# Optimization experiments

Measured on AMD Instinct MI355X. Metric: run time of the kernel, lower is better.

## Reference

```python
import jax, jax.numpy as jnp
import numpy as np
import math

NUM_LANDMARKS = 64
HEAD_DIM = 64
NUM_HEAD = 16
BATCH = 4
SEQ_LEN = 4096


def iterative_inv(mat, n_iter=6):
    # mat: [..., m, m]
    I = jnp.eye(mat.shape[-1], dtype=mat.dtype)
    K = mat
    # scalar normalization: global max of column sums * global max of row sums
    scale = 1.0 / (jnp.max(jnp.sum(jnp.abs(K), axis=-2)) * jnp.max(jnp.sum(jnp.abs(K), axis=-1)))
    V = scale * jnp.swapaxes(K, -1, -2)
    for _ in range(n_iter):
        KV = jnp.matmul(K, V)
        V = jnp.matmul(0.25 * V, 13.0 * I - jnp.matmul(KV, 15.0 * I - jnp.matmul(KV, 7.0 * I - KV)))
    return V


def setup_inputs() -> dict:
    key = jax.random.key(0)
    k1, k2, k3 = jax.random.split(key, 3)
    shape = (BATCH, NUM_HEAD, SEQ_LEN, HEAD_DIM)
    Q = jax.random.normal(k1, shape, dtype=jnp.float32)
    K = jax.random.normal(k2, shape, dtype=jnp.float32)
    V = jax.random.normal(k3, shape, dtype=jnp.float32)
    return {"Q": Q, "K": K, "V": V}


def reference(Q, K, V):
    seq_len = Q.shape[-2]
    m = NUM_LANDMARKS
    scale = 1.0 / math.sqrt(math.sqrt(HEAD_DIM))
    Q = Q * scale
    K = K * scale
    # landmark pooling: mean over contiguous segments of length seq_len // m
    seg = seq_len // m
    Q_lm = Q.reshape(-1, NUM_HEAD, m, seg, HEAD_DIM).mean(axis=-2)  # [B,H,m,d]
    K_lm = K.reshape(-1, NUM_HEAD, m, seg, HEAD_DIM).mean(axis=-2)  # [B,H,m,d]
    # three softmax kernels
    kernel_1 = jax.nn.softmax(jnp.einsum('bhsd,bhmd->bhsm', Q, K_lm), axis=-1)   # [B,H,S,m]
    kernel_2 = jax.nn.softmax(jnp.einsum('bhmd,bhnd->bhmn', Q_lm, K_lm), axis=-1)  # [B,H,m,m]
    kernel_3 = jax.nn.softmax(jnp.einsum('bhmd,bhsd->bhms', Q_lm, K), axis=-1)   # [B,H,m,S]
    inv_k2 = iterative_inv(kernel_2)
    X = jnp.matmul(jnp.matmul(kernel_1, inv_k2), jnp.matmul(kernel_3, V))  # [B,H,S,d]
    return X
```

## Files before the change

### kernel.cpp

```cpp
#include <hip/hip_runtime.h>
#include <hip/hip_bf16.h>

#define PAD 68
#define KP  72
#define SCALE 0.35355339059327379f

typedef __attribute__((ext_vector_type(8))) short bf16x8;
typedef __attribute__((ext_vector_type(4))) float f32x4;
#define MFMA_BF16 __builtin_amdgcn_mfma_f32_16x16x32_bf16

__device__ __forceinline__ short f2b(float f) {
    unsigned u = __float_as_uint(f);
    u += 0x7fff + ((u >> 16) & 1);
    return (short)(u >> 16);
}
__device__ __forceinline__ float b2f(short h) {
    return __uint_as_float(((unsigned)(unsigned short)h) << 16);
}

__device__ __forceinline__ void fma16(float acc[16], float a, const float* b) {
    const float4* b4 = reinterpret_cast<const float4*>(b);
    float4 x0 = b4[0], x1 = b4[1], x2 = b4[2], x3 = b4[3];
    acc[0]  += a * x0.x; acc[1]  += a * x0.y; acc[2]  += a * x0.z; acc[3]  += a * x0.w;
    acc[4]  += a * x1.x; acc[5]  += a * x1.y; acc[6]  += a * x1.z; acc[7]  += a * x1.w;
    acc[8]  += a * x2.x; acc[9]  += a * x2.y; acc[10] += a * x2.z; acc[11] += a * x2.w;
    acc[12] += a * x3.x; acc[13] += a * x3.y; acc[14] += a * x3.z; acc[15] += a * x3.w;
}

__device__ __forceinline__ int SWI(int row, int colS) {
    return (((row << 7) + (colS << 1)) ^ ((row & 7) << 4)) >> 1;
}

__global__ __launch_bounds__(256) void pool_kernel(const float* __restrict__ Q,
                                                   const float* __restrict__ K,
                                                   float* __restrict__ Qlm,
                                                   float* __restrict__ Klm,
                                                   short* __restrict__ Qlm_b,
                                                   short* __restrict__ Klm_b) {
    __shared__ float4 red[256];
    const int blk = blockIdx.x;
    const int t = threadIdx.x;
    const int d4 = t & 15;
    const int rg = t >> 4;
    const float4* Q4 = reinterpret_cast<const float4*>(Q);
    const float4* K4 = reinterpret_cast<const float4*>(K);

    float4 sQ = {0.f, 0.f, 0.f, 0.f}, sK = {0.f, 0.f, 0.f, 0.f};
#pragma unroll
    for (int rr = 0; rr < 4; rr++) {
        int row = blk * 64 + rg * 4 + rr;
        int off4 = (row << 4) + d4;
        float4 q = Q4[off4], k = K4[off4];
        sQ.x += q.x; sQ.y += q.y; sQ.z += q.z; sQ.w += q.w;
        sK.x += k.x; sK.y += k.y; sK.z += k.z; sK.w += k.w;
    }
    const float c = SCALE * (1.0f / 64.0f);
    red[t] = sQ;
    __syncthreads();
    if (t < 16) {
        float4 s = {0.f, 0.f, 0.f, 0.f};
#pragma unroll
        for (int g = 0; g < 16; g++) {
            float4 v = red[g * 16 + t];
            s.x += v.x; s.y += v.y; s.z += v.z; s.w += v.w;
        }
        s.x *= c; s.y *= c; s.z *= c; s.w *= c;
        reinterpret_cast<float4*>(Qlm + blk * 64)[t] = s;
        ushort4 ub = { (unsigned short)f2b(s.x), (unsigned short)f2b(s.y),
                       (unsigned short)f2b(s.z), (unsigned short)f2b(s.w) };
        *reinterpret_cast<ushort4*>(&Qlm_b[blk * 64 + t * 4]) = ub;
    }
    __syncthreads();
    red[t] = sK;
    __syncthreads();
    if (t < 16) {
        float4 s = {0.f, 0.f, 0.f, 0.f};
#pragma unroll
        for (int g = 0; g < 16; g++) {
            float4 v = red[g * 16 + t];
            s.x += v.x; s.y += v.y; s.z += v.z; s.w += v.w;
        }
        s.x *= c; s.y *= c; s.z *= c; s.w *= c;
        reinterpret_cast<float4*>(Klm + blk * 64)[t] = s;
        ushort4 ub = { (unsigned short)f2b(s.x), (unsigned short)f2b(s.y),
                       (unsigned short)f2b(s.z), (unsigned short)f2b(s.w) };
        *reinterpret_cast<ushort4*>(&Klm_b[blk * 64 + t * 4]) = ub;
    }
}

__global__ __launch_bounds__(256) void k2_kernel(const float* __restrict__ Qlm,
                                                 const float* __restrict__ Klm,
                                                 float* __restrict__ K2g,
                                                 unsigned* __restrict__ colmax) {
    __shared__ float Ql[64 * PAD], Kl[64 * PAD], S2[64 * PAD];
    const int bh = blockIdx.x, t = threadIdx.x;
#pragma unroll
    for (int n = 0; n < 16; n++) {
        int f = t + n * 256;
        Ql[(f >> 6) * PAD + (f & 63)] = Qlm[bh * 4096 + f];
        Kl[(f >> 6) * PAD + (f & 63)] = Klm[bh * 4096 + f];
    }
    __syncthreads();
    const int i = t >> 2, j0 = (t & 3) * 16;
    float acc[16];
#pragma unroll
    for (int u = 0; u < 16; u++) acc[u] = 0.f;
    const float4* Ql4 = reinterpret_cast<const float4*>(Ql);
    const float4* Kl4 = reinterpret_cast<const float4*>(Kl);
    for (int k4 = 0; k4 < 16; k4++) {
        float4 a = Ql4[i * 17 + k4];
#pragma unroll
        for (int u = 0; u < 16; u++) {
            float4 b = Kl4[(j0 + u) * 17 + k4];
            acc[u] += a.x * b.x + a.y * b.y + a.z * b.z + a.w * b.w;
        }
    }
#pragma unroll
    for (int u = 0; u < 16; u++) S2[i * PAD + j0 + u] = acc[u];
    __syncthreads();
    if (t < 64) {
        float m = -1e30f;
        for (int j = 0; j < 64; j++) m = fmaxf(m, S2[t * PAD + j]);
        float sum = 0.f;
        for (int j = 0; j < 64; j++) {
            float e = __expf(S2[t * PAD + j] - m);
            S2[t * PAD + j] = e; sum += e;
        }
        float inv = 1.0f / sum;
        for (int j = 0; j < 64; j++) S2[t * PAD + j] *= inv;
    }
    __syncthreads();
#pragma unroll
    for (int n = 0; n < 16; n++) {
        int f = t + n * 256;
        K2g[bh * 4096 + f] = S2[(f >> 6) * PAD + (f & 63)];
    }
    if (t < 64) {
        float c = 0.f;
        for (int ii = 0; ii < 64; ii++) c += S2[ii * PAD + t];
        atomicMax(colmax, __float_as_uint(c));
    }
}

__global__ __launch_bounds__(256) void fused_inv_k3v(const short* __restrict__ Qlm_b,
                                                     const float* __restrict__ K,
                                                     const float* __restrict__ V,
                                                     float* __restrict__ W2acc,
                                                     float* __restrict__ rowsum3,
                                                     const float* __restrict__ K2g,
                                                     const unsigned* __restrict__ colmax,
                                                     float* __restrict__ K2invg) {
    __shared__ __align__(16) char smem[65536];
    const int t = threadIdx.x;
    const int w = t >> 6, lane = t & 63, quad = lane >> 4, l15 = lane & 15;

    if (blockIdx.x < 64) {
        short* Krh = reinterpret_cast<short*>(smem);
        short* Krl = Krh + 4096;
        short* Ath = Krl + 4096;
        short* Atl = Ath + 4096;
        short* B1h = Atl + 4096;
        short* B1l = B1h + 4096;
        short* B2h = B1l + 4096;
        short* B2l = B2h + 4096;
        const int bh = blockIdx.x;
        const float scv = 1.0f / __uint_as_float(*colmax);
        const float* Kg = K2g + bh * 4096;

#pragma unroll
        for (int n = 0; n < 4; n++) {
            int f4 = t + n * 256;
            int r = f4 >> 4, c0 = (f4 & 15) * 4;
            float4 kk = *reinterpret_cast<const float4*>(Kg + r * 64 + c0);
            short h0 = f2b(kk.x), h1 = f2b(kk.y), h2 = f2b(kk.z), h3 = f2b(kk.w);
            ushort4 uh = {(unsigned short)h0, (unsigned short)h1,
                          (unsigned short)h2, (unsigned short)h3};
            ushort4 ul = {(unsigned short)f2b(kk.x - b2f(h0)), (unsigned short)f2b(kk.y - b2f(h1)),
                          (unsigned short)f2b(kk.z - b2f(h2)), (unsigned short)f2b(kk.w - b2f(h3))};
            *reinterpret_cast<ushort4*>(&Krh[SWI(r, c0)]) = uh;
            *reinterpret_cast<ushort4*>(&Krl[SWI(r, c0)]) = ul;
            float s0 = scv * kk.x, s1 = scv * kk.y, s2 = scv * kk.z, s3 = scv * kk.w;
            short g0 = f2b(s0), g1 = f2b(s1), g2 = f2b(s2), g3 = f2b(s3);
            ushort4 vh = {(unsigned short)g0, (unsigned short)g1,
                          (unsigned short)g2, (unsigned short)g3};
            ushort4 vl = {(unsigned short)f2b(s0 - b2f(g0)), (unsigned short)f2b(s1 - b2f(g1)),
                          (unsigned short)f2b(s2 - b2f(g2)), (unsigned short)f2b(s3 - b2f(g3))};
            *reinterpret_cast<ushort4*>(&B1h[SWI(r, c0)]) = vh;
            *reinterpret_cast<ushort4*>(&B1l[SWI(r, c0)]) = vl;
            float t0 = scv * Kg[(c0 + 0) * 64 + r];
            float t1 = scv * Kg[(c0 + 1) * 64 + r];
            float t2 = scv * Kg[(c0 + 2) * 64 + r];
            float t3 = scv * Kg[(c0 + 3) * 64 + r];
            short e0 = f2b(t0), e1 = f2b(t1), e2 = f2b(t2), e3 = f2b(t3);
            ushort4 th = {(unsigned short)e0, (unsigned short)e1,
                          (unsigned short)e2, (unsigned short)e3};
            ushort4 tl = {(unsigned short)f2b(t0 - b2f(e0)), (unsigned short)f2b(t1 - b2f(e1)),
                          (unsigned short)f2b(t2 - b2f(e2)), (unsigned short)f2b(t3 - b2f(e3))};
            *reinterpret_cast<ushort4*>(&B2h[SWI(r, c0)]) = th;
            *reinterpret_cast<ushort4*>(&B2l[SWI(r, c0)]) = tl;
        }
        float vreg[4][4];
#pragma unroll
        for (int nt = 0; nt < 4; nt++) {
            float4 vv = *reinterpret_cast<const float4*>(
                Kg + (nt * 16 + l15) * 64 + w * 16 + quad * 4);
            vreg[nt][0] = scv * vv.x; vreg[nt][1] = scv * vv.y;
            vreg[nt][2] = scv * vv.z; vreg[nt][3] = scv * vv.w;
        }
        __syncthreads();

#define LOADA(Lh, Ll) \
        bf16x8 ah0 = *reinterpret_cast<const bf16x8*>(&Lh[SWI(w * 16 + l15, quad * 8)]); \
        bf16x8 ah1 = *reinterpret_cast<const bf16x8*>(&Lh[SWI(w * 16 + l15, quad * 8 + 32)]); \
        bf16x8 al0 = *reinterpret_cast<const bf16x8*>(&Ll[SWI(w * 16 + l15, quad * 8)]); \
        bf16x8 al1 = *reinterpret_cast<const bf16x8*>(&Ll[SWI(w * 16 + l15, quad * 8 + 32)]);
#define PRODNT(Bh, Bl, nt, c) { \
        bf16x8 bh0 = *reinterpret_cast<const bf16x8*>(&Bh[SWI(nt * 16 + l15, quad * 8)]); \
        bf16x8 bh1 = *reinterpret_cast<const bf16x8*>(&Bh[SWI(nt * 16 + l15, quad * 8 + 32)]); \
        bf16x8 bl0 = *reinterpret_cast<const bf16x8*>(&Bl[SWI(nt * 16 + l15, quad * 8)]); \
        bf16x8 bl1 = *reinterpret_cast<const bf16x8*>(&Bl[SWI(nt * 16 + l15, quad * 8 + 32)]); \
        c = MFMA_BF16(ah0, bh0, c, 0, 0, 0); c = MFMA_BF16(ah1, bh1, c, 0, 0, 0); \
        c = MFMA_BF16(ah0, bl0, c, 0, 0, 0); c = MFMA_BF16(ah1, bl1, c, 0, 0, 0); \
        c = MFMA_BF16(al0, bh0, c, 0, 0, 0); c = MFMA_BF16(al1, bh1, c, 0, 0, 0); \
        c = MFMA_BF16(al0, bl0, c, 0, 0, 0); c = MFMA_BF16(al1, bl1, c, 0, 0, 0); }

        for (int iter = 0; iter < 6; iter++) {
            {
                LOADA(Krh, Krl)
#pragma unroll
                for (int nt = 0; nt < 4; nt++) {
                    f32x4 c = {0.f, 0.f, 0.f, 0.f};
                    PRODNT(B1h, B1l, nt, c)
                    short h0 = f2b(c[0]), h1 = f2b(c[1]), h2 = f2b(c[2]), h3 = f2b(c[3]);
                    ushort4 uh = {(unsigned short)h0, (unsigned short)h1,
                                  (unsigned short)h2, (unsigned short)h3};
                    ushort4 ul = {(unsigned short)f2b(c[0] - b2f(h0)),
                                  (unsigned short)f2b(c[1] - b2f(h1)),
                                  (unsigned short)f2b(c[2] - b2f(h2)),
                                  (unsigned short)f2b(c[3] - b2f(h3))};
                    *reinterpret_cast<ushort4*>(&Ath[SWI(nt * 16 + l15, w * 16 + quad * 4)]) = uh;
                    *reinterpret_cast<ushort4*>(&Atl[SWI(nt * 16 + l15, w * 16 + quad * 4)]) = ul;
                }
            }
            __syncthreads();
            float p[4][4];
            {
                LOADA(B2h, B2l)
#pragma unroll
                for (int nt = 0; nt < 4; nt++) {
                    f32x4 c = {0.f, 0.f, 0.f, 0.f};
                    PRODNT(Ath, Atl, nt, c)
#pragma unroll
                    for (int reg = 0; reg < 4; reg++) {
                        p[nt][reg] = c[reg];
                        short hh = f2b(c[reg]);
                        B1h[SWI(w * 16 + quad * 4 + reg, nt * 16 + l15)] = hh;
                        B1l[SWI(w * 16 + quad * 4 + reg, nt * 16 + l15)] = f2b(c[reg] - b2f(hh));
                    }
                }
            }
            __syncthreads();
            float q[4][4];
            {
                LOADA(B1h, B1l)
#pragma unroll
                for (int nt = 0; nt < 4; nt++) {
                    f32x4 c = {0.f, 0.f, 0.f, 0.f};
                    PRODNT(Ath, Atl, nt, c)
#pragma unroll
                    for (int reg = 0; reg < 4; reg++) {
                        q[nt][reg] = c[reg];
                        short hh = f2b(c[reg]);
                        B2h[SWI(w * 16 + quad * 4 + reg, nt * 16 + l15)] = hh;
                        B2l[SWI(w * 16 + quad * 4 + reg, nt * 16 + l15)] = f2b(c[reg] - b2f(hh));
                    }
                }
            }
            __syncthreads();
            {
                LOADA(B2h, B2l)
#pragma unroll
                for (int nt = 0; nt < 4; nt++) {
                    f32x4 c = {0.f, 0.f, 0.f, 0.f};
                    PRODNT(Ath, Atl, nt, c)
#pragma unroll
                    for (int reg = 0; reg < 4; reg++)
                        vreg[nt][reg] = 0.25f * (13.f * vreg[nt][reg] - 15.f * p[nt][reg]
                                                 + 7.f * q[nt][reg] - c[reg]);
                }
            }
#pragma unroll
            for (int nt = 0; nt < 4; nt++) {
                short h0 = f2b(vreg[nt][0]), h1 = f2b(vreg[nt][1]);
                short h2 = f2b(vreg[nt][2]), h3 = f2b(vreg[nt][3]);
                short g0 = f2b(vreg[nt][0] - b2f(h0)), g1 = f2b(vreg[nt][1] - b2f(h1));
                short g2 = f2b(vreg[nt][2] - b2f(h2)), g3 = f2b(vreg[nt][3] - b2f(h3));
                ushort4 uh = {(unsigned short)h0, (unsigned short)h1,
                              (unsigned short)h2, (unsigned short)h3};
                ushort4 ul = {(unsigned short)g0, (unsigned short)g1,
                              (unsigned short)g2, (unsigned short)g3};
                *reinterpret_cast<ushort4*>(&B1h[SWI(nt * 16 + l15, w * 16 + quad * 4)]) = uh;
                *reinterpret_cast<ushort4*>(&B1l[SWI(nt * 16 + l15, w * 16 + quad * 4)]) = ul;
                B2h[SWI(w * 16 + quad * 4 + 0, nt * 16 + l15)] = h0;
                B2h[SWI(w * 16 + quad * 4 + 1, nt * 16 + l15)] = h1;
                B2h[SWI(w * 16 + quad * 4 + 2, nt * 16 + l15)] = h2;
                B2h[SWI(w * 16 + quad * 4 + 3, nt * 16 + l15)] = h3;
                B2l[SWI(w * 16 + quad * 4 + 0, nt * 16 + l15)] = g0;
                B2l[SWI(w * 16 + quad * 4 + 1, nt * 16 + l15)] = g1;
                B2l[SWI(w * 16 + quad * 4 + 2, nt * 16 + l15)] = g2;
                B2l[SWI(w * 16 + quad * 4 + 3, nt * 16 + l15)] = g3;
            }
            __syncthreads();
        }
#undef LOADA
#undef PRODNT
#pragma unroll
        for (int nt = 0; nt < 4; nt++)
#pragma unroll
            for (int reg = 0; reg < 4; reg++)
                K2invg[bh * 4096 + (w * 16 + quad * 4 + reg) * 64 + nt * 16 + l15] =
                    vreg[nt][reg];
        return;
    }

    short* Kt = reinterpret_cast<short*>(smem);
    short* Vt = Kt + 64 * KP;
    short* Eb = Vt + 64 * KP;
    const int idx = blockIdx.x - 64;
    const int chunk = idx & 31, bh = idx >> 5;
    const float4* K4 = reinterpret_cast<const float4*>(K);
    const float4* V4 = reinterpret_cast<const float4*>(V);
    const int dg = t & 15;
    const int kr = t >> 4;
    const int bhBase = bh * 4096;

    const bf16x8* Qb = reinterpret_cast<const bf16x8*>(Qlm_b + bh * 4096);
    bf16x8 a0 = Qb[(w * 16 + l15) * 8 + quad];
    bf16x8 a1 = Qb[(w * 16 + l15) * 8 + quad + 4];

    f32x4 oacc[4];
    float rsum[4];
#pragma unroll
    for (int nt = 0; nt < 4; nt++) { oacc[nt] = (f32x4){0.f, 0.f, 0.f, 0.f}; rsum[nt] = 0.f; }

    const int sb0 = chunk * 128;
    for (int tile = 0; tile < 2; tile++) {
        const int sb = sb0 + tile * 64;
        __syncthreads();
#pragma unroll
        for (int n = 0; n < 4; n++) {
            float4 kk = K4[(bhBase + sb + kr + 16 * n) * 16 + dg];
            ushort4 uk = { (unsigned short)f2b(SCALE * kk.x), (unsigned short)f2b(SCALE * kk.y),
                           (unsigned short)f2b(SCALE * kk.z), (unsigned short)f2b(SCALE * kk.w) };
            *reinterpret_cast<ushort4*>(&Kt[(kr + 16 * n) * KP + dg * 4]) = uk;
        }
        {
            float4 pv0 = V4[(bhBase + sb + kr * 4 + 0) * 16 + dg];
            float4 pv1 = V4[(bhBase + sb + kr * 4 + 1) * 16 + dg];
            float4 pv2 = V4[(bhBase + sb + kr * 4 + 2) * 16 + dg];
            float4 pv3 = V4[(bhBase + sb + kr * 4 + 3) * 16 + dg];
            ushort4 u0 = { (unsigned short)f2b(pv0.x), (unsigned short)f2b(pv1.x),
                           (unsigned short)f2b(pv2.x), (unsigned short)f2b(pv3.x) };
            ushort4 u1 = { (unsigned short)f2b(pv0.y), (unsigned short)f2b(pv1.y),
                           (unsigned short)f2b(pv2.y), (unsigned short)f2b(pv3.y) };
            ushort4 u2 = { (unsigned short)f2b(pv0.z), (unsigned short)f2b(pv1.z),
                           (unsigned short)f2b(pv2.z), (unsigned short)f2b(pv3.z) };
            ushort4 u3 = { (unsigned short)f2b(pv0.w), (unsigned short)f2b(pv1.w),
                           (unsigned short)f2b(pv2.w), (unsigned short)f2b(pv3.w) };
            *reinterpret_cast<ushort4*>(&Vt[(dg * 4 + 0) * KP + kr * 4]) = u0;
            *reinterpret_cast<ushort4*>(&Vt[(dg * 4 + 1) * KP + kr * 4]) = u1;
            *reinterpret_cast<ushort4*>(&Vt[(dg * 4 + 2) * KP + kr * 4]) = u2;
            *reinterpret_cast<ushort4*>(&Vt[(dg * 4 + 3) * KP + kr * 4]) = u3;
        }
        __syncthreads();
#pragma unroll
        for (int nt = 0; nt < 4; nt++) {
            bf16x8 b0 = *reinterpret_cast<const bf16x8*>(&Kt[(nt * 16 + l15) * KP + quad * 8]);
            bf16x8 b1 = *reinterpret_cast<const bf16x8*>(&Kt[(nt * 16 + l15) * KP + quad * 8 + 32]);
            f32x4 c = {0.f, 0.f, 0.f, 0.f};
            c = MFMA_BF16(a0, b0, c, 0, 0, 0);
            c = MFMA_BF16(a1, b1, c, 0, 0, 0);
#pragma unroll
            for (int reg = 0; reg < 4; reg++) {
                float e = __expf(c[reg]);
                rsum[reg] += e;
                Eb[(w * 16 + quad * 4 + reg) * KP + nt * 16 + l15] = f2b(e);
            }
        }
        bf16x8 e0 = *reinterpret_cast<const bf16x8*>(&Eb[(w * 16 + l15) * KP + quad * 8]);
        bf16x8 e1 = *reinterpret_cast<const bf16x8*>(&Eb[(w * 16 + l15) * KP + quad * 8 + 32]);
#pragma unroll
        for (int nt = 0; nt < 4; nt++) {
            bf16x8 b0 = *reinterpret_cast<const bf16x8*>(&Vt[(nt * 16 + l15) * KP + quad * 8]);
            bf16x8 b1 = *reinterpret_cast<const bf16x8*>(&Vt[(nt * 16 + l15) * KP + quad * 8 + 32]);
            oacc[nt] = MFMA_BF16(e0, b0, oacc[nt], 0, 0, 0);
            oacc[nt] = MFMA_BF16(e1, b1, oacc[nt], 0, 0, 0);
        }
    }
#pragma unroll
    for (int reg = 0; reg < 4; reg++) {
        float s = rsum[reg];
        s += __shfl_xor(s, 1); s += __shfl_xor(s, 2);
        s += __shfl_xor(s, 4); s += __shfl_xor(s, 8);
        rsum[reg] = s;
    }
    const int row0 = w * 16 + quad * 4;
    if (l15 == 0) {
#pragma unroll
        for (int reg = 0; reg < 4; reg++)
            atomicAdd(&rowsum3[bh * 64 + row0 + reg], rsum[reg]);
    }
#pragma unroll
    for (int nt = 0; nt < 4; nt++)
#pragma unroll
        for (int reg = 0; reg < 4; reg++)
            atomicAdd(&W2acc[(bh * 64 + row0 + reg) * 64 + nt * 16 + l15], oacc[nt][reg]);
}

__global__ __launch_bounds__(256) void wmid_kernel(const float* __restrict__ K2invg,
                                                   const float* __restrict__ W2acc,
                                                   const float* __restrict__ rowsum3,
                                                   short* __restrict__ Wth,
                                                   short* __restrict__ Wtl) {
    __shared__ float I1[64 * PAD], W2[64 * PAD];
    const int bh = blockIdx.x, t = threadIdx.x;
#pragma unroll
    for (int n = 0; n < 16; n++) {
        int f = t + n * 256;
        int r = f >> 6;
        I1[r * PAD + (f & 63)] = K2invg[bh * 4096 + f];
        W2[r * PAD + (f & 63)] = W2acc[bh * 4096 + f] / rowsum3[bh * 64 + r];
    }
    __syncthreads();
    const int i = t >> 2, j0 = (t & 3) * 16;
    float acc[16];
#pragma unroll
    for (int u = 0; u < 16; u++) acc[u] = 0.f;
    for (int k = 0; k < 64; k++) fma16(acc, I1[i * PAD + k], W2 + k * PAD + j0);
#pragma unroll
    for (int u = 0; u < 16; u++) {
        float wv = acc[u];
        short hi = f2b(wv);
        short lo = f2b(wv - b2f(hi));
        Wth[bh * 4096 + (j0 + u) * 64 + i] = hi;
        Wtl[bh * 4096 + (j0 + u) * 64 + i] = lo;
    }
}

__global__ __launch_bounds__(256) void final_mfma(const float* __restrict__ Q,
                                                  const short* __restrict__ Klm_b,
                                                  const short* __restrict__ Wth,
                                                  const short* __restrict__ Wtl,
                                                  float* __restrict__ out) {
    __shared__ short Eb[64 * KP];
    const int sc = blockIdx.x, bh = blockIdx.y, t = threadIdx.x;
    const int w = t >> 6, lane = t & 63, quad = lane >> 4, l15 = lane & 15;
    const int s0 = sc * 64;
    const int row = w * 16 + l15;

    const float* qrow = Q + ((size_t)bh * 4096 + s0 + row) * 64 + quad * 8;
    float4 qa = *reinterpret_cast<const float4*>(qrow);
    float4 qb = *reinterpret_cast<const float4*>(qrow + 4);
    float4 qc = *reinterpret_cast<const float4*>(qrow + 32);
    float4 qd = *reinterpret_cast<const float4*>(qrow + 36);

    const bf16x8* Kb = reinterpret_cast<const bf16x8*>(Klm_b + bh * 4096);
    const bf16x8* Hb = reinterpret_cast<const bf16x8*>(Wth + bh * 4096);
    const bf16x8* Lb = reinterpret_cast<const bf16x8*>(Wtl + bh * 4096);

    bf16x8 a0, a1;
    a0[0] = f2b(SCALE * qa.x); a0[1] = f2b(SCALE * qa.y);
    a0[2] = f2b(SCALE * qa.z); a0[3] = f2b(SCALE * qa.w);
    a0[4] = f2b(SCALE * qb.x); a0[5] = f2b(SCALE * qb.y);
    a0[6] = f2b(SCALE * qb.z); a0[7] = f2b(SCALE * qb.w);
    a1[0] = f2b(SCALE * qc.x); a1[1] = f2b(SCALE * qc.y);
    a1[2] = f2b(SCALE * qc.z); a1[3] = f2b(SCALE * qc.w);
    a1[4] = f2b(SCALE * qd.x); a1[5] = f2b(SCALE * qd.y);
    a1[6] = f2b(SCALE * qd.z); a1[7] = f2b(SCALE * qd.w);

    float rsum[4] = {0.f, 0.f, 0.f, 0.f};
#pragma unroll
    for (int nt = 0; nt < 4; nt++) {
        bf16x8 b0 = Kb[(nt * 16 + l15) * 8 + quad];
        bf16x8 b1 = Kb[(nt * 16 + l15) * 8 + quad + 4];
        f32x4 c = {0.f, 0.f, 0.f, 0.f};
        c = MFMA_BF16(a0, b0, c, 0, 0, 0);
        c = MFMA_BF16(a1, b1, c, 0, 0, 0);
#pragma unroll
        for (int reg = 0; reg < 4; reg++) {
            float e = __expf(c[reg]);
            rsum[reg] += e;
            Eb[(w * 16 + quad * 4 + reg) * KP + nt * 16 + l15] = f2b(e);
        }
    }
#pragma unroll
    for (int reg = 0; reg < 4; reg++) {
        float s = rsum[reg];
        s += __shfl_xor(s, 1); s += __shfl_xor(s, 2);
        s += __shfl_xor(s, 4); s += __shfl_xor(s, 8);
        rsum[reg] = 1.0f / s;
    }
    bf16x8 e0 = *reinterpret_cast<const bf16x8*>(&Eb[row * KP + quad * 8]);
    bf16x8 e1 = *reinterpret_cast<const bf16x8*>(&Eb[row * KP + quad * 8 + 32]);
    const int row0 = w * 16 + quad * 4;
#pragma unroll
    for (int nt = 0; nt < 4; nt++) {
        bf16x8 bh0 = Hb[(nt * 16 + l15) * 8 + quad];
        bf16x8 bh1 = Hb[(nt * 16 + l15) * 8 + quad + 4];
        bf16x8 bl0 = Lb[(nt * 16 + l15) * 8 + quad];
        bf16x8 bl1 = Lb[(nt * 16 + l15) * 8 + quad + 4];
        f32x4 c = {0.f, 0.f, 0.f, 0.f};
        c = MFMA_BF16(e0, bh0, c, 0, 0, 0);
        c = MFMA_BF16(e1, bh1, c, 0, 0, 0);
        c = MFMA_BF16(e0, bl0, c, 0, 0, 0);
        c = MFMA_BF16(e1, bl1, c, 0, 0, 0);
#pragma unroll
        for (int reg = 0; reg < 4; reg++)
            out[((size_t)bh * 4096 + s0 + row0 + reg) * 64 + nt * 16 + l15] = c[reg] * rsum[reg];
    }
}

extern "C" void kernel_launch(void* const* d_in, const int* in_sizes, int n_in,
                              void* d_out, int out_size, void* d_ws, size_t ws_size,
                              hipStream_t stream) {
    const float* Q = (const float*)d_in[0];
    const float* K = (const float*)d_in[1];
    const float* V = (const float*)d_in[2];
    float* out = (float*)d_out;
    float* ws = (float*)d_ws;

    float* Qlm     = ws;
    float* Klm     = ws + 262144;
    float* K2      = ws + 524288;
    float* K2inv   = ws + 786432;
    short* Wth     = (short*)(ws + 1048576);
    short* Wtl     = (short*)(ws + 1179648);
    float* W2acc   = ws + 1310720;
    float* rowsum3 = ws + 1572864;
    unsigned* colmax = (unsigned*)(ws + 1576960);
    short* Qlm_b   = (short*)(ws + 1576964);
    short* Klm_b   = (short*)(ws + 1708036);

    hipMemsetAsync(W2acc, 0, (262144 + 4096 + 1) * sizeof(float), stream);

    pool_kernel<<<4096, 256, 0, stream>>>(Q, K, Qlm, Klm, Qlm_b, Klm_b);
    k2_kernel<<<64, 256, 0, stream>>>(Qlm, Klm, K2, colmax);
    fused_inv_k3v<<<2112, 256, 0, stream>>>(Qlm_b, K, V, W2acc, rowsum3, K2, colmax, K2inv);
    wmid_kernel<<<64, 256, 0, stream>>>(K2inv, W2acc, rowsum3, Wth, Wtl);
    final_mfma<<<dim3(64, 64), 256, 0, stream>>>(Q, Klm_b, Wth, Wtl, out);
}
```

Before: 313.7 us.

## Move k2 and wmid matmuls to split-bf16 MFMA; batch four row tiles per final block

The small 64x64 matmuls in k2_kernel and wmid_kernel now run on bf16 MFMA instructions instead of scalar fp32 FMAs. Inputs are split into hi/lo bf16 pairs and three cross-products are summed to stay close to fp32 accuracy. The pooling kernel now writes hi/lo bf16 landmark copies in place of fp32 arrays. final_mfma processes four 64-row tiles per block with prefetched Q and K-landmark fragments held in registers across tiles, cutting the grid fourfold and setting an occupancy hint of 4. The risks are lower parallelism in the final kernel and small numerical differences from the split-bf16 approximation.

```diff
diff --git a/kernel.cpp b/kernel.cpp
--- a/kernel.cpp
+++ b/kernel.cpp
@@ -1,7 +1,6 @@
 #include <hip/hip_runtime.h>
 #include <hip/hip_bf16.h>
 
-#define PAD 68
 #define KP  72
 #define SCALE 0.35355339059327379f
 
@@ -18,25 +17,16 @@
     return __uint_as_float(((unsigned)(unsigned short)h) << 16);
 }
 
-__device__ __forceinline__ void fma16(float acc[16], float a, const float* b) {
-    const float4* b4 = reinterpret_cast<const float4*>(b);
-    float4 x0 = b4[0], x1 = b4[1], x2 = b4[2], x3 = b4[3];
-    acc[0]  += a * x0.x; acc[1]  += a * x0.y; acc[2]  += a * x0.z; acc[3]  += a * x0.w;
-    acc[4]  += a * x1.x; acc[5]  += a * x1.y; acc[6]  += a * x1.z; acc[7]  += a * x1.w;
-    acc[8]  += a * x2.x; acc[9]  += a * x2.y; acc[10] += a * x2.z; acc[11] += a * x2.w;
-    acc[12] += a * x3.x; acc[13] += a * x3.y; acc[14] += a * x3.z; acc[15] += a * x3.w;
-}
-
 __device__ __forceinline__ int SWI(int row, int colS) {
     return (((row << 7) + (colS << 1)) ^ ((row & 7) << 4)) >> 1;
 }
 
 __global__ __launch_bounds__(256) void pool_kernel(const float* __restrict__ Q,
                                                    const float* __restrict__ K,
-                                                   float* __restrict__ Qlm,
-                                                   float* __restrict__ Klm,
-                                                   short* __restrict__ Qlm_b,
-                                                   short* __restrict__ Klm_b) {
+                                                   short* __restrict__ Qlm_bh,
+                                                   short* __restrict__ Qlm_bl,
+                                                   short* __restrict__ Klm_bh,
+                                                   short* __restrict__ Klm_bl) {
     __shared__ float4 red[256];
     const int blk = blockIdx.x;
     const int t = threadIdx.x;
@@ -65,10 +55,13 @@
             s.x += v.x; s.y += v.y; s.z += v.z; s.w += v.w;
         }
         s.x *= c; s.y *= c; s.z *= c; s.w *= c;
-        reinterpret_cast<float4*>(Qlm + blk * 64)[t] = s;
-        ushort4 ub = { (unsigned short)f2b(s.x), (unsigned short)f2b(s.y),
-                       (unsigned short)f2b(s.z), (unsigned short)f2b(s.w) };
-        *reinterpret_cast<ushort4*>(&Qlm_b[blk * 64 + t * 4]) = ub;
+        short h0 = f2b(s.x), h1 = f2b(s.y), h2 = f2b(s.z), h3 = f2b(s.w);
+        ushort4 uh = {(unsigned short)h0, (unsigned short)h1,
+                      (unsigned short)h2, (unsigned short)h3};
+        ushort4 ul = {(unsigned short)f2b(s.x - b2f(h0)), (unsigned short)f2b(s.y - b2f(h1)),
+                      (unsigned short)f2b(s.z - b2f(h2)), (unsigned short)f2b(s.w - b2f(h3))};
+        *reinterpret_cast<ushort4*>(&Qlm_bh[blk * 64 + t * 4]) = uh;
+        *reinterpret_cast<ushort4*>(&Qlm_bl[blk * 64 + t * 4]) = ul;
     }
     __syncthreads();
     red[t] = sK;
@@ -81,68 +74,93 @@
             s.x += v.x; s.y += v.y; s.z += v.z; s.w += v.w;
         }
         s.x *= c; s.y *= c; s.z *= c; s.w *= c;
-        reinterpret_cast<float4*>(Klm + blk * 64)[t] = s;
-        ushort4 ub = { (unsigned short)f2b(s.x), (unsigned short)f2b(s.y),
-                       (unsigned short)f2b(s.z), (unsigned short)f2b(s.w) };
-        *reinterpret_cast<ushort4*>(&Klm_b[blk * 64 + t * 4]) = ub;
-    }
-}
-
-__global__ __launch_bounds__(256) void k2_kernel(const float* __restrict__ Qlm,
-                                                 const float* __restrict__ Klm,
+        short h0 = f2b(s.x), h1 = f2b(s.y), h2 = f2b(s.z), h3 = f2b(s.w);
+        ushort4 uh = {(unsigned short)h0, (unsigned short)h1,
+                      (unsigned short)h2, (unsigned short)h3};
+        ushort4 ul = {(unsigned short)f2b(s.x - b2f(h0)), (unsigned short)f2b(s.y - b2f(h1)),
+                      (unsigned short)f2b(s.z - b2f(h2)), (unsigned short)f2b(s.w - b2f(h3))};
+        *reinterpret_cast<ushort4*>(&Klm_bh[blk * 64 + t * 4]) = uh;
+        *reinterpret_cast<ushort4*>(&Klm_bl[blk * 64 + t * 4]) = ul;
+    }
+}
+
+__global__ __launch_bounds__(256) void k2_kernel(const short* __restrict__ Qlm_bh,
+                                                 const short* __restrict__ Qlm_bl,
+                                                 const short* __restrict__ Klm_bh,
+                                                 const short* __restrict__ Klm_bl,
                                                  float* __restrict__ K2g,
                                                  unsigned* __restrict__ colmax) {
-    __shared__ float Ql[64 * PAD], Kl[64 * PAD], S2[64 * PAD];
+    __shared__ float csum[16 * 64];
     const int bh = blockIdx.x, t = threadIdx.x;
-#pragma unroll
-    for (int n = 0; n < 16; n++) {
-        int f = t + n * 256;
-        Ql[(f >> 6) * PAD + (f & 63)] = Qlm[bh * 4096 + f];
-        Kl[(f >> 6) * PAD + (f & 63)] = Klm[bh * 4096 + f];
-    }
-    __syncthreads();
-    const int i = t >> 2, j0 = (t & 3) * 16;
-    float acc[16];
-#pragma unroll
-    for (int u = 0; u < 16; u++) acc[u] = 0.f;
-    const float4* Ql4 = reinterpret_cast<const float4*>(Ql);
-    const float4* Kl4 = reinterpret_cast<const float4*>(Kl);
-    for (int k4 = 0; k4 < 16; k4++) {
-        float4 a = Ql4[i * 17 + k4];
-#pragma unroll
-        for (int u = 0; u < 16; u++) {
-            float4 b = Kl4[(j0 + u) * 17 + k4];
-            acc[u] += a.x * b.x + a.y * b.y + a.z * b.z + a.w * b.w;
-        }
-    }
-#pragma unroll
-    for (int u = 0; u < 16; u++) S2[i * PAD + j0 + u] = acc[u];
+    const int w = t >> 6, lane = t & 63, quad = lane >> 4, l15 = lane & 15;
+
+    const bf16x8* Ah = reinterpret_cast<const bf16x8*>(Qlm_bh + bh * 4096);
+    const bf16x8* Al = reinterpret_cast<const bf16x8*>(Qlm_bl + bh * 4096);
+    const bf16x8* Bh = reinterpret_cast<const bf16x8*>(Klm_bh + bh * 4096);
+    const bf16x8* Bl = reinterpret_cast<const bf16x8*>(Klm_bl + bh * 4096);
+    bf16x8 ah0 = Ah[(w * 16 + l15) * 8 + quad], ah1 = Ah[(w * 16 + l15) * 8 + quad + 4];
+    bf16x8 al0 = Al[(w * 16 + l15) * 8 + quad], al1 = Al[(w * 16 + l15) * 8 + quad + 4];
+
+    f32x4 c[4];
+#pragma unroll
+    for (int nt = 0; nt < 4; nt++) {
+        bf16x8 bh0 = Bh[(nt * 16 + l15) * 8 + quad], bh1 = Bh[(nt * 16 + l15) * 8 + quad + 4];
+        bf16x8 bl0 = Bl[(nt * 16 + l15) * 8 + quad], bl1 = Bl[(nt * 16 + l15) * 8 + quad + 4];
+        f32x4 cc = {0.f, 0.f, 0.f, 0.f};
+        cc = MFMA_BF16(ah0, bh0, cc, 0, 0, 0); cc = MFMA_BF16(ah1, bh1, cc, 0, 0, 0);
+        cc = MFMA_BF16(ah0, bl0, cc, 0, 0, 0); cc = MFMA_BF16(ah1, bl1, cc, 0, 0, 0);
+        cc = MFMA_BF16(al0, bh0, cc, 0, 0, 0); cc = MFMA_BF16(al1, bh1, cc, 0, 0, 0);
+        c[nt] = cc;
+    }
+    float m[4] = {-1e30f, -1e30f, -1e30f, -1e30f};
+#pragma unroll
+    for (int nt = 0; nt < 4; nt++)
+#pragma unroll
+        for (int reg = 0; reg < 4; reg++) m[reg] = fmaxf(m[reg], c[nt][reg]);
+#pragma unroll
+    for (int reg = 0; reg < 4; reg++) {
+        float v = m[reg];
+        v = fmaxf(v, __shfl_xor(v, 1)); v = fmaxf(v, __shfl_xor(v, 2));
+        v = fmaxf(v, __shfl_xor(v, 4)); v = fmaxf(v, __shfl_xor(v, 8));
+        m[reg] = v;
+    }
+    float e[4][4];
+    float rs[4] = {0.f, 0.f, 0.f, 0.f};
+#pragma unroll
+    for (int nt = 0; nt < 4; nt++)
+#pragma unroll
+        for (int reg = 0; reg < 4; reg++) {
+            float ev = __expf(c[nt][reg] - m[reg]);
+            e[nt][reg] = ev; rs[reg] += ev;
+        }
+#pragma unroll
+    for (int reg = 0; reg < 4; reg++) {
+        float v = rs[reg];
+        v += __shfl_xor(v, 1); v += __shfl_xor(v, 2);
+        v += __shfl_xor(v, 4); v += __shfl_xor(v, 8);
+        rs[reg] = 1.0f / v;
+    }
+    float ps[4] = {0.f, 0.f, 0.f, 0.f};
+#pragma unroll
+    for (int nt = 0; nt < 4; nt++) {
+#pragma unroll
+        for (int reg = 0; reg < 4; reg++) {
+            float p = e[nt][reg] * rs[reg];
+            K2g[bh * 4096 + (w * 16 + quad * 4 + reg) * 64 + nt * 16 + l15] = p;
+            ps[nt] += p;
+        }
+        csum[(w * 4 + quad) * 64 + nt * 16 + l15] = ps[nt];
+    }
     __syncthreads();
     if (t < 64) {
-        float m = -1e30f;
-        for (int j = 0; j < 64; j++) m = fmaxf(m, S2[t * PAD + j]);
-        float sum = 0.f;
-        for (int j = 0; j < 64; j++) {
-            float e = __expf(S2[t * PAD + j] - m);
-            S2[t * PAD + j] = e; sum += e;
-        }
-        float inv = 1.0f / sum;
-        for (int j = 0; j < 64; j++) S2[t * PAD + j] *= inv;
-    }
-    __syncthreads();
-#pragma unroll
-    for (int n = 0; n < 16; n++) {
-        int f = t + n * 256;
-        K2g[bh * 4096 + f] = S2[(f >> 6) * PAD + (f & 63)];
-    }
-    if (t < 64) {
-        float c = 0.f;
-        for (int ii = 0; ii < 64; ii++) c += S2[ii * PAD + t];
-        atomicMax(colmax, __float_as_uint(c));
-    }
-}
-
-__global__ __launch_bounds__(256) void fused_inv_k3v(const short* __restrict__ Qlm_b,
+        float s = 0.f;
+#pragma unroll
+        for (int i = 0; i < 16; i++) s += csum[i * 64 + t];
+        atomicMax(colmax, __float_as_uint(s));
+    }
+}
+
+__global__ __launch_bounds__(256) void fused_inv_k3v(const short* __restrict__ Qlm_bh,
                                                      const float* __restrict__ K,
                                                      const float* __restrict__ V,
                                                      float* __restrict__ W2acc,
@@ -334,7 +352,7 @@
     const int kr = t >> 4;
     const int bhBase = bh * 4096;
 
-    const bf16x8* Qb = reinterpret_cast<const bf16x8*>(Qlm_b + bh * 4096);
+    const bf16x8* Qb = reinterpret_cast<const bf16x8*>(Qlm_bh + bh * 4096);
     bf16x8 a0 = Qb[(w * 16 + l15) * 8 + quad];
     bf16x8 a1 = Qb[(w * 16 + l15) * 8 + quad + 4];
 
@@ -422,101 +440,140 @@
                                                    const float* __restrict__ rowsum3,
                                                    short* __restrict__ Wth,
                                                    short* __restrict__ Wtl) {
-    __shared__ float I1[64 * PAD], W2[64 * PAD];
+    __shared__ short W2th[4096], W2tl[4096];
     const int bh = blockIdx.x, t = threadIdx.x;
-#pragma unroll
-    for (int n = 0; n < 16; n++) {
-        int f = t + n * 256;
-        int r = f >> 6;
-        I1[r * PAD + (f & 63)] = K2invg[bh * 4096 + f];
-        W2[r * PAD + (f & 63)] = W2acc[bh * 4096 + f] / rowsum3[bh * 64 + r];
+    const int w = t >> 6, lane = t & 63, quad = lane >> 4, l15 = lane & 15;
+
+#pragma unroll
+    for (int n16 = 0; n16 < 16; n16++) {
+        int f = t + n16 * 256;
+        int k = f >> 6, n = f & 63;
+        float v = W2acc[bh * 4096 + k * 64 + n] / rowsum3[bh * 64 + k];
+        short hi = f2b(v);
+        W2th[SWI(n, k)] = hi;
+        W2tl[SWI(n, k)] = f2b(v - b2f(hi));
+    }
+    const float* Ar = K2invg + bh * 4096 + (w * 16 + l15) * 64;
+    float4 x0 = *reinterpret_cast<const float4*>(Ar + quad * 8);
+    float4 x1 = *reinterpret_cast<const float4*>(Ar + quad * 8 + 4);
+    float4 x2 = *reinterpret_cast<const float4*>(Ar + quad * 8 + 32);
+    float4 x3 = *reinterpret_cast<const float4*>(Ar + quad * 8 + 36);
+    bf16x8 ah0, al0, ah1, al1;
+    {
+        float a[8] = {x0.x, x0.y, x0.z, x0.w, x1.x, x1.y, x1.z, x1.w};
+        float b[8] = {x2.x, x2.y, x2.z, x2.w, x3.x, x3.y, x3.z, x3.w};
+#pragma unroll
+        for (int i = 0; i < 8; i++) {
+            short h = f2b(a[i]); ah0[i] = h; al0[i] = f2b(a[i] - b2f(h));
+            short g = f2b(b[i]); ah1[i] = g; al1[i] = f2b(b[i] - b2f(g));
+        }
     }
     __syncthreads();
-    const int i = t >> 2, j0 = (t & 3) * 16;
-    float acc[16];
-#pragma unroll
-    for (int u = 0; u < 16; u++) acc[u] = 0.f;
-    for (int k = 0; k < 64; k++) fma16(acc, I1[i * PAD + k], W2 + k * PAD + j0);
-#pragma unroll
-    for (int u = 0; u < 16; u++) {
-        float wv = acc[u];
-        short hi = f2b(wv);
-        short lo = f2b(wv - b2f(hi));
-        Wth[bh * 4096 + (j0 + u) * 64 + i] = hi;
-        Wtl[bh * 4096 + (j0 + u) * 64 + i] = lo;
-    }
-}
-
-__global__ __launch_bounds__(256) void final_mfma(const float* __restrict__ Q,
-                                                  const short* __restrict__ Klm_b,
-                                                  const short* __restrict__ Wth,
-                                                  const short* __restrict__ Wtl,
-                                                  float* __restrict__ out) {
+#pragma unroll
+    for (int nt = 0; nt < 4; nt++) {
+        bf16x8 bh0 = *reinterpret_cast<const bf16x8*>(&W2th[SWI(nt * 16 + l15, quad * 8)]);
+        bf16x8 bh1 = *reinterpret_cast<const bf16x8*>(&W2th[SWI(nt * 16 + l15, quad * 8 + 32)]);
+        bf16x8 bl0 = *reinterpret_cast<const bf16x8*>(&W2tl[SWI(nt * 16 + l15, quad * 8)]);
+        bf16x8 bl1 = *reinterpret_cast<const bf16x8*>(&W2tl[SWI(nt * 16 + l15, quad * 8 + 32)]);
+        f32x4 cc = {0.f, 0.f, 0.f, 0.f};
+        cc = MFMA_BF16(ah0, bh0, cc, 0, 0, 0); cc = MFMA_BF16(ah1, bh1, cc, 0, 0, 0);
+        cc = MFMA_BF16(ah0, bl0, cc, 0, 0, 0); cc = MFMA_BF16(ah1, bl1, cc, 0, 0, 0);
+        cc = MFMA_BF16(al0, bh0, cc, 0, 0, 0); cc = MFMA_BF16(al1, bh1, cc, 0, 0, 0);
+#pragma unroll
+        for (int reg = 0; reg < 4; reg++) {
+            float wv = cc[reg];
+            short hi = f2b(wv);
+            int col = nt * 16 + l15, r = w * 16 + quad * 4 + reg;
+            Wth[bh * 4096 + col * 64 + r] = hi;
+            Wtl[bh * 4096 + col * 64 + r] = f2b(wv - b2f(hi));
+        }
+    }
+}
+
+__global__ __launch_bounds__(256, 4) void final_mfma(const float* __restrict__ Q,
+                                                     const short* __restrict__ Klm_b,
+                                                     const short* __restrict__ Wth,
+                                                     const short* __restrict__ Wtl,
+                                                     float* __restrict__ out) {
     __shared__ short Eb[64 * KP];
     const int sc = blockIdx.x, bh = blockIdx.y, t = threadIdx.x;
     const int w = t >> 6, lane = t & 63, quad = lane >> 4, l15 = lane & 15;
-    const int s0 = sc * 64;
     const int row = w * 16 + l15;
 
-    const float* qrow = Q + ((size_t)bh * 4096 + s0 + row) * 64 + quad * 8;
-    float4 qa = *reinterpret_cast<const float4*>(qrow);
-    float4 qb = *reinterpret_cast<const float4*>(qrow + 4);
-    float4 qc = *reinterpret_cast<const float4*>(qrow + 32);
-    float4 qd = *reinterpret_cast<const float4*>(qrow + 36);
-
     const bf16x8* Kb = reinterpret_cast<const bf16x8*>(Klm_b + bh * 4096);
+    bf16x8 kb[4][2];
+#pragma unroll
+    for (int nt = 0; nt < 4; nt++) {
+        kb[nt][0] = Kb[(nt * 16 + l15) * 8 + quad];
+        kb[nt][1] = Kb[(nt * 16 + l15) * 8 + quad + 4];
+    }
     const bf16x8* Hb = reinterpret_cast<const bf16x8*>(Wth + bh * 4096);
     const bf16x8* Lb = reinterpret_cast<const bf16x8*>(Wtl + bh * 4096);
 
-    bf16x8 a0, a1;
-    a0[0] = f2b(SCALE * qa.x); a0[1] = f2b(SCALE * qa.y);
-    a0[2] = f2b(SCALE * qa.z); a0[3] = f2b(SCALE * qa.w);
-    a0[4] = f2b(SCALE * qb.x); a0[5] = f2b(SCALE * qb.y);
-    a0[6] = f2b(SCALE * qb.z); a0[7] = f2b(SCALE * qb.w);
-    a1[0] = f2b(SCALE * qc.x); a1[1] = f2b(SCALE * qc.y);
-    a1[2] = f2b(SCALE * qc.z); a1[3] = f2b(SCALE * qc.w);
-    a1[4] = f2b(SCALE * qd.x); a1[5] = f2b(SCALE * qd.y);
-    a1[6] = f2b(SCALE * qd.z); a1[7] = f2b(SCALE * qd.w);
-
-    float rsum[4] = {0.f, 0.f, 0.f, 0.f};
-#pragma unroll
-    for (int nt = 0; nt < 4; nt++) {
-        bf16x8 b0 = Kb[(nt * 16 + l15) * 8 + quad];
-        bf16x8 b1 = Kb[(nt * 16 + l15) * 8 + quad + 4];
-        f32x4 c = {0.f, 0.f, 0.f, 0.f};
-        c = MFMA_BF16(a0, b0, c, 0, 0, 0);
-        c = MFMA_BF16(a1, b1, c, 0, 0, 0);
+    const size_t qbase = ((size_t)bh * 4096 + sc * 256 + row) * 64 + quad * 8;
+    float4 qa = *reinterpret_cast<const float4*>(Q + qbase);
+    float4 qb = *reinterpret_cast<const float4*>(Q + qbase + 4);
+    float4 qc = *reinterpret_cast<const float4*>(Q + qbase + 32);
+    float4 qd = *reinterpret_cast<const float4*>(Q + qbase + 36);
+
+#pragma unroll
+    for (int st = 0; st < 4; st++) {
+        bf16x8 a0, a1;
+        a0[0] = f2b(SCALE * qa.x); a0[1] = f2b(SCALE * qa.y);
+        a0[2] = f2b(SCALE * qa.z); a0[3] = f2b(SCALE * qa.w);
+        a0[4] = f2b(SCALE * qb.x); a0[5] = f2b(SCALE * qb.y);
+        a0[6] = f2b(SCALE * qb.z); a0[7] = f2b(SCALE * qb.w);
+        a1[0] = f2b(SCALE * qc.x); a1[1] = f2b(SCALE * qc.y);
+        a1[2] = f2b(SCALE * qc.z); a1[3] = f2b(SCALE * qc.w);
+        a1[4] = f2b(SCALE * qd.x); a1[5] = f2b(SCALE * qd.y);
+        a1[6] = f2b(SCALE * qd.z); a1[7] = f2b(SCALE * qd.w);
+        if (st < 3) {
+            const float* np = Q + qbase + (size_t)(st + 1) * 4096;
+            qa = *reinterpret_cast<const float4*>(np);
+            qb = *reinterpret_cast<const float4*>(np + 4);
+            qc = *reinterpret_cast<const float4*>(np + 32);
+            qd = *reinterpret_cast<const float4*>(np + 36);
+        }
+        float rsum[4] = {0.f, 0.f, 0.f, 0.f};
+#pragma unroll
+        for (int nt = 0; nt < 4; nt++) {
+            f32x4 c = {0.f, 0.f, 0.f, 0.f};
+            c = MFMA_BF16(a0, kb[nt][0], c, 0, 0, 0);
+            c = MFMA_BF16(a1, kb[nt][1], c, 0, 0, 0);
+#pragma unroll
+            for (int reg = 0; reg < 4; reg++) {
+                float e = __expf(c[reg]);
+                rsum[reg] += e;
+                Eb[(w * 16 + quad * 4 + reg) * KP + nt * 16 + l15] = f2b(e);
+            }
+        }
 #pragma unroll
         for (int reg = 0; reg < 4; reg++) {
-            float e = __expf(c[reg]);
-            rsum[reg] += e;
-            Eb[(w * 16 + quad * 4 + reg) * KP + nt * 16 + l15] = f2b(e);
-        }
-    }
-#pragma unroll
-    for (int reg = 0; reg < 4; reg++) {
-        float s = rsum[reg];
-        s += __shfl_xor(s, 1); s += __shfl_xor(s, 2);
-        s += __shfl_xor(s, 4); s += __shfl_xor(s, 8);
-        rsum[reg] = 1.0f / s;
-    }
-    bf16x8 e0 = *reinterpret_cast<const bf16x8*>(&Eb[row * KP + quad * 8]);
-    bf16x8 e1 = *reinterpret_cast<const bf16x8*>(&Eb[row * KP + quad * 8 + 32]);
-    const int row0 = w * 16 + quad * 4;
-#pragma unroll
-    for (int nt = 0; nt < 4; nt++) {
-        bf16x8 bh0 = Hb[(nt * 16 + l15) * 8 + quad];
-        bf16x8 bh1 = Hb[(nt * 16 + l15) * 8 + quad + 4];
-        bf16x8 bl0 = Lb[(nt * 16 + l15) * 8 + quad];
-        bf16x8 bl1 = Lb[(nt * 16 + l15) * 8 + quad + 4];
-        f32x4 c = {0.f, 0.f, 0.f, 0.f};
-        c = MFMA_BF16(e0, bh0, c, 0, 0, 0);
-        c = MFMA_BF16(e1, bh1, c, 0, 0, 0);
-        c = MFMA_BF16(e0, bl0, c, 0, 0, 0);
-        c = MFMA_BF16(e1, bl1, c, 0, 0, 0);
-#pragma unroll
-        for (int reg = 0; reg < 4; reg++)
-            out[((size_t)bh * 4096 + s0 + row0 + reg) * 64 + nt * 16 + l15] = c[reg] * rsum[reg];
+            float s = rsum[reg];
+            s += __shfl_xor(s, 1); s += __shfl_xor(s, 2);
+            s += __shfl_xor(s, 4); s += __shfl_xor(s, 8);
+            rsum[reg] = 1.0f / s;
+        }
+        bf16x8 e0 = *reinterpret_cast<const bf16x8*>(&Eb[row * KP + quad * 8]);
+        bf16x8 e1 = *reinterpret_cast<const bf16x8*>(&Eb[row * KP + quad * 8 + 32]);
+        const int row0 = w * 16 + quad * 4;
+        const int s0 = sc * 256 + st * 64;
+#pragma unroll
+        for (int nt = 0; nt < 4; nt++) {
+            bf16x8 bh0 = Hb[(nt * 16 + l15) * 8 + quad];
+            bf16x8 bh1 = Hb[(nt * 16 + l15) * 8 + quad + 4];
+            bf16x8 bl0 = Lb[(nt * 16 + l15) * 8 + quad];
+            bf16x8 bl1 = Lb[(nt * 16 + l15) * 8 + quad + 4];
+            f32x4 c = {0.f, 0.f, 0.f, 0.f};
+            c = MFMA_BF16(e0, bh0, c, 0, 0, 0);
+            c = MFMA_BF16(e1, bh1, c, 0, 0, 0);
+            c = MFMA_BF16(e0, bl0, c, 0, 0, 0);
+            c = MFMA_BF16(e1, bl1, c, 0, 0, 0);
+#pragma unroll
+            for (int reg = 0; reg < 4; reg++)
+                out[((size_t)bh * 4096 + s0 + row0 + reg) * 64 + nt * 16 + l15] =
+                    c[reg] * rsum[reg];
+        }
     }
 }
 
@@ -529,23 +586,23 @@
     float* out = (float*)d_out;
     float* ws = (float*)d_ws;
 
-    float* Qlm     = ws;
-    float* Klm     = ws + 262144;
-    float* K2      = ws + 524288;
-    float* K2inv   = ws + 786432;
-    short* Wth     = (short*)(ws + 1048576);
-    short* Wtl     = (short*)(ws + 1179648);
-    float* W2acc   = ws + 1310720;
-    float* rowsum3 = ws + 1572864;
-    unsigned* colmax = (unsigned*)(ws + 1576960);
-    short* Qlm_b   = (short*)(ws + 1576964);
-    short* Klm_b   = (short*)(ws + 1708036);
+    float* K2      = ws;
+    float* K2inv   = ws + 262144;
+    float* W2acc   = ws + 524288;
+    float* rowsum3 = ws + 786432;
+    unsigned* colmax = (unsigned*)(ws + 790528);
+    short* Qlm_bh  = (short*)(ws + 790532);
+    short* Qlm_bl  = Qlm_bh + 262144;
+    short* Klm_bh  = Qlm_bl + 262144;
+    short* Klm_bl  = Klm_bh + 262144;
+    short* Wth     = Klm_bl + 262144;
+    short* Wtl     = Wth + 262144;
 
     hipMemsetAsync(W2acc, 0, (262144 + 4096 + 1) * sizeof(float), stream);
 
-    pool_kernel<<<4096, 256, 0, stream>>>(Q, K, Qlm, Klm, Qlm_b, Klm_b);
-    k2_kernel<<<64, 256, 0, stream>>>(Qlm, Klm, K2, colmax);
-    fused_inv_k3v<<<2112, 256, 0, stream>>>(Qlm_b, K, V, W2acc, rowsum3, K2, colmax, K2inv);
+    pool_kernel<<<4096, 256, 0, stream>>>(Q, K, Qlm_bh, Qlm_bl, Klm_bh, Klm_bl);
+    k2_kernel<<<64, 256, 0, stream>>>(Qlm_bh, Qlm_bl, Klm_bh, Klm_bl, K2, colmax);
+    fused_inv_k3v<<<2112, 256, 0, stream>>>(Qlm_bh, K, V, W2acc, rowsum3, K2, colmax, K2inv);
     wmid_kernel<<<64, 256, 0, stream>>>(K2inv, W2acc, rowsum3, Wth, Wtl);
-    final_mfma<<<dim3(64, 64), 256, 0, stream>>>(Q, Klm_b, Wth, Wtl, out);
-}
+    final_mfma<<<dim3(16, 64), 256, 0, stream>>>(Q, Klm_bh, Wth, Wtl, out);
+}
```

After: 299.5 us. -4.5%, faster.
